# Optimization experiments

Hardware: AMD Instinct MI355X
Metric: run time of the kernel (lower is better)

Reference implementation:

```python
import jax, jax.numpy as jnp
import numpy as np

VOCAB = 50257
C = 8  # n_dim_categories
B, T = 4, 4096


def setup_inputs() -> dict:
    key = jax.random.key(0)
    k1, k2, k3 = jax.random.split(key, 3)
    token_ids = jax.random.randint(k1, (B, T), 0, VOCAB)
    dim_embedding = jax.random.normal(k2, (VOCAB, C), dtype=jnp.float32)
    compatibility = jax.random.normal(k3, (C, C), dtype=jnp.float32) * 0.1
    return {"token_ids": token_ids, "dim_embedding": dim_embedding,
            "compatibility": compatibility}


def reference(token_ids, dim_embedding, compatibility):
    # (B,T,C): embedding lookup then softmax over categories
    dim_probs = jax.nn.softmax(dim_embedding[token_ids], axis=-1)
    # bilinear compatibility over all T x T token pairs -> (B,T,T)
    compat = jnp.einsum('btc,cd,bsd->bts', dim_probs, compatibility, dim_probs)
    mask_bias = jax.nn.sigmoid(compat) * 2 - 1
    return mask_bias
```

## Files before the change

### kernel.cpp

```cpp
#include <hip/hip_runtime.h>
#include <hip/hip_bf16.h>

typedef float f32x4 __attribute__((ext_vector_type(4)));

namespace {
constexpr int kB = 4;
constexpr int kT = 4096;
constexpr int kC = 8;
constexpr int kN = kB * kT;
constexpr int kTRows = 32;
constexpr int kSPerThread = 4;
constexpr int kBlockThreads = 256;
constexpr int kSTile = kBlockThreads * kSPerThread;
}

__global__ __launch_bounds__(64) void dam_prep(const int* __restrict__ token_ids,
                                               const float* __restrict__ emb,
                                               const float* __restrict__ cmat,
                                               float* __restrict__ p_ws,
                                               float* __restrict__ z_ws) {
    int tid = blockIdx.x * blockDim.x + threadIdx.x;
    if (tid >= kN) return;
    int tok = token_ids[tid];
    const f32x4* row = reinterpret_cast<const f32x4*>(emb) + (size_t)tok * 2;
    f32x4 e0 = row[0], e1 = row[1];
    float e[kC] = {e0.x, e0.y, e0.z, e0.w, e1.x, e1.y, e1.z, e1.w};
    float m = e[0];
#pragma unroll
    for (int i = 1; i < kC; ++i) m = fmaxf(m, e[i]);
    float p[kC], sum = 0.f;
#pragma unroll
    for (int i = 0; i < kC; ++i) { p[i] = __expf(e[i] - m); sum += p[i]; }
    float inv = 1.0f / sum;
#pragma unroll
    for (int i = 0; i < kC; ++i) p[i] *= inv;
    float z[kC];
#pragma unroll
    for (int c = 0; c < kC; ++c) {
        float acc = 0.f;
#pragma unroll
        for (int d = 0; d < kC; ++d) acc = fmaf(cmat[c * kC + d], p[d], acc);
        z[c] = -acc;
    }
    f32x4* po = reinterpret_cast<f32x4*>(p_ws) + (size_t)tid * 2;
    po[0] = f32x4{p[0], p[1], p[2], p[3]};
    po[1] = f32x4{p[4], p[5], p[6], p[7]};
    f32x4* zo = reinterpret_cast<f32x4*>(z_ws) + (size_t)tid * 2;
    zo[0] = f32x4{z[0], z[1], z[2], z[3]};
    zo[1] = f32x4{z[4], z[5], z[6], z[7]};
}

__global__ __launch_bounds__(256) void dam_mask(const float* __restrict__ p_ws,
                                                const float* __restrict__ z_ws,
                                                float* __restrict__ out) {
    const int b = blockIdx.z;
    const int t0 = blockIdx.y * kTRows;
    const int s0 = blockIdx.x * kSTile;
    __shared__ f32x4 p_lds[kTRows * 2];
    const int tid = threadIdx.x;
    if (tid < kTRows * 2)
        p_lds[tid] = reinterpret_cast<const f32x4*>(p_ws + ((size_t)(b * kT + t0)) * kC)[tid];
    __syncthreads();

    const int s = s0 + tid * kSPerThread;
    const f32x4* zr = reinterpret_cast<const f32x4*>(z_ws) + ((size_t)(b * kT) + s) * 2;
    float z[kSPerThread][kC];
#pragma unroll
    for (int j = 0; j < kSPerThread; ++j) {
        f32x4 a = zr[j * 2 + 0];
        f32x4 c = zr[j * 2 + 1];
        z[j][0] = a.x; z[j][1] = a.y; z[j][2] = a.z; z[j][3] = a.w;
        z[j][4] = c.x; z[j][5] = c.y; z[j][6] = c.z; z[j][7] = c.w;
    }

    float* orow = out + ((size_t)(b * kT + t0)) * kT + s;
#pragma unroll
    for (int tt = 0; tt < kTRows; ++tt) {
        f32x4 p0 = p_lds[tt * 2 + 0];
        f32x4 p1 = p_lds[tt * 2 + 1];
        float pr[kC] = {p0.x, p0.y, p0.z, p0.w, p1.x, p1.y, p1.z, p1.w};
        float r[kSPerThread];
#pragma unroll
        for (int j = 0; j < kSPerThread; ++j) {
            float acc = 0.f;
#pragma unroll
            for (int i = 0; i < kC; ++i) acc = fmaf(pr[i], z[j][i], acc);
            float ex = __expf(acc);
            r[j] = (1.f - ex) * __builtin_amdgcn_rcpf(1.f + ex);
        }
        f32x4 ov = {r[0], r[1], r[2], r[3]};
        *reinterpret_cast<f32x4*>(orow + (size_t)tt * kT) = ov;
    }
}

extern "C" void kernel_launch(void* const* d_in, const int* in_sizes, int n_in,
                              void* d_out, int out_size, void* d_ws, size_t ws_size,
                              hipStream_t stream) {
    const int* token_ids = (const int*)d_in[0];
    const float* emb     = (const float*)d_in[1];
    const float* cmat    = (const float*)d_in[2];
    float* out  = (float*)d_out;
    float* p_ws = (float*)d_ws;
    float* z_ws = p_ws + (size_t)kN * kC;

    dam_prep<<<kN / 64, 64, 0, stream>>>(token_ids, emb, cmat, p_ws, z_ws);
    dim3 grid(kT / kSTile, kT / kTRows, kB);
    dam_mask<<<grid, kBlockThreads, 0, stream>>>(p_ws, z_ws, out);
}
```

Before: 53.49 us.

## Restructure mask kernel to stream full rows per wave with z prefetch

Each wavefront now owns two output rows and walks across all columns in 256-wide chunks, keeping both rows' probability vectors in registers and prefetching the next chunk of z into registers. This drops the LDS staging and the block barrier, and each z load is reused for two rows. The catch is that z is reread per row pair instead of being reused across 32 rows per block, so L2 traffic goes up. The grid also gets fewer, longer-running blocks. The kernel is bound by output writes, so the effect depends mostly on store throughput.

```diff
diff --git a/kernel.cpp b/kernel.cpp
--- a/kernel.cpp
+++ b/kernel.cpp
@@ -8,10 +8,10 @@
 constexpr int kT = 4096;
 constexpr int kC = 8;
 constexpr int kN = kB * kT;
-constexpr int kTRows = 32;
-constexpr int kSPerThread = 4;
+constexpr int kTRowsPB = 8;
+constexpr int kSChunk = 256;
+constexpr int kNChunks = kT / kSChunk;
 constexpr int kBlockThreads = 256;
-constexpr int kSTile = kBlockThreads * kSPerThread;
 }
 
 __global__ __launch_bounds__(64) void dam_prep(const int* __restrict__ token_ids,
@@ -53,43 +53,54 @@
 __global__ __launch_bounds__(256) void dam_mask(const float* __restrict__ p_ws,
                                                 const float* __restrict__ z_ws,
                                                 float* __restrict__ out) {
-    const int b = blockIdx.z;
-    const int t0 = blockIdx.y * kTRows;
-    const int s0 = blockIdx.x * kSTile;
-    __shared__ f32x4 p_lds[kTRows * 2];
+    const int b = blockIdx.y;
+    const int t0 = blockIdx.x * kTRowsPB;
     const int tid = threadIdx.x;
-    if (tid < kTRows * 2)
-        p_lds[tid] = reinterpret_cast<const f32x4*>(p_ws + ((size_t)(b * kT + t0)) * kC)[tid];
-    __syncthreads();
+    const int wid = tid >> 6;
+    const int lane = tid & 63;
+    const int r0 = t0 + wid * 2;
 
-    const int s = s0 + tid * kSPerThread;
-    const f32x4* zr = reinterpret_cast<const f32x4*>(z_ws) + ((size_t)(b * kT) + s) * 2;
-    float z[kSPerThread][kC];
+    const f32x4* pp = reinterpret_cast<const f32x4*>(p_ws) + ((size_t)(b * kT + r0)) * 2;
+    f32x4 pa0 = pp[0], pa1 = pp[1], pb0 = pp[2], pb1 = pp[3];
+    float pr0[kC] = {pa0.x, pa0.y, pa0.z, pa0.w, pa1.x, pa1.y, pa1.z, pa1.w};
+    float pr1[kC] = {pb0.x, pb0.y, pb0.z, pb0.w, pb1.x, pb1.y, pb1.z, pb1.w};
+
+    const f32x4* zbase = reinterpret_cast<const f32x4*>(z_ws) + (size_t)(b * kT) * 2;
+
+    f32x4 zc[8], zn[8];
 #pragma unroll
-    for (int j = 0; j < kSPerThread; ++j) {
-        f32x4 a = zr[j * 2 + 0];
-        f32x4 c = zr[j * 2 + 1];
-        z[j][0] = a.x; z[j][1] = a.y; z[j][2] = a.z; z[j][3] = a.w;
-        z[j][4] = c.x; z[j][5] = c.y; z[j][6] = c.z; z[j][7] = c.w;
-    }
+    for (int k = 0; k < 8; ++k) zc[k] = zbase[(size_t)lane * 8 + k];
 
-    float* orow = out + ((size_t)(b * kT + t0)) * kT + s;
+    float* orow0 = out + ((size_t)(b * kT + r0)) * kT;
+    float* orow1 = orow0 + kT;
+
+    for (int it = 0; it < kNChunks; ++it) {
+        if (it + 1 < kNChunks) {
+            const f32x4* znext = zbase + ((size_t)(it + 1) * kSChunk + lane * 4) * 2;
 #pragma unroll
-    for (int tt = 0; tt < kTRows; ++tt) {
-        f32x4 p0 = p_lds[tt * 2 + 0];
-        f32x4 p1 = p_lds[tt * 2 + 1];
-        float pr[kC] = {p0.x, p0.y, p0.z, p0.w, p1.x, p1.y, p1.z, p1.w};
-        float r[kSPerThread];
+            for (int k = 0; k < 8; ++k) zn[k] = znext[k];
+        }
+        float r0v[4], r1v[4];
 #pragma unroll
-        for (int j = 0; j < kSPerThread; ++j) {
-            float acc = 0.f;
+        for (int j = 0; j < 4; ++j) {
+            f32x4 a = zc[j * 2 + 0];
+            f32x4 c = zc[j * 2 + 1];
+            float zv[kC] = {a.x, a.y, a.z, a.w, c.x, c.y, c.z, c.w};
+            float acc0 = 0.f, acc1 = 0.f;
 #pragma unroll
-            for (int i = 0; i < kC; ++i) acc = fmaf(pr[i], z[j][i], acc);
-            float ex = __expf(acc);
-            r[j] = (1.f - ex) * __builtin_amdgcn_rcpf(1.f + ex);
+            for (int i = 0; i < kC; ++i) {
+                acc0 = fmaf(pr0[i], zv[i], acc0);
+                acc1 = fmaf(pr1[i], zv[i], acc1);
+            }
+            float e0 = __expf(acc0), e1 = __expf(acc1);
+            r0v[j] = (1.f - e0) * __builtin_amdgcn_rcpf(1.f + e0);
+            r1v[j] = (1.f - e1) * __builtin_amdgcn_rcpf(1.f + e1);
         }
-        f32x4 ov = {r[0], r[1], r[2], r[3]};
-        *reinterpret_cast<f32x4*>(orow + (size_t)tt * kT) = ov;
+        const int col = it * kSChunk + lane * 4;
+        *reinterpret_cast<f32x4*>(orow0 + col) = f32x4{r0v[0], r0v[1], r0v[2], r0v[3]};
+        *reinterpret_cast<f32x4*>(orow1 + col) = f32x4{r1v[0], r1v[1], r1v[2], r1v[3]};
+#pragma unroll
+        for (int k = 0; k < 8; ++k) zc[k] = zn[k];
     }
 }
 
@@ -104,6 +115,6 @@
     float* z_ws = p_ws + (size_t)kN * kC;
 
     dam_prep<<<kN / 64, 64, 0, stream>>>(token_ids, emb, cmat, p_ws, z_ws);
-    dim3 grid(kT / kSTile, kT / kTRows, kB);
+    dim3 grid(kT / kTRowsPB, kB);
     dam_mask<<<grid, kBlockThreads, 0, stream>>>(p_ws, z_ws, out);
 }
```

New measurement: 134.2 us. 2.51x slower.
